# Performance work log

Hardware: AMD Instinct MI355X
Metric: run time of the kernel (lower is better)

Reference implementation:

```python
import jax, jax.numpy as jnp
import numpy as np

DOWNSAMPLE = 1

def _meshgrid(oh, ow):
    # grid rows: x in [-1,1] repeated per row, y in [-1,1] per column, ones -> [3, oh*ow]
    x_t = jnp.tile(jnp.linspace(-1.0, 1.0, ow, dtype=jnp.float32)[None, :], (oh, 1))
    y_t = jnp.tile(jnp.linspace(-1.0, 1.0, oh, dtype=jnp.float32)[:, None], (1, ow))
    ones = jnp.ones((1, oh * ow), dtype=jnp.float32)
    return jnp.concatenate([x_t.reshape(1, -1), y_t.reshape(1, -1), ones], axis=0)

def setup_inputs() -> dict:
    key = jax.random.key(0)
    k1, k2 = jax.random.split(key)
    B, C, H, W = 32, 16, 256, 256
    inp = jax.random.normal(k1, (B, C, H, W), dtype=jnp.float32)
    # theta near identity with noise so sampling is non-degenerate
    ident = jnp.array([1.0, 0.0, 0.0, 0.0, 1.0, 0.0], dtype=jnp.float32)
    theta = ident[None, :] + 0.1 * jax.random.normal(k2, (B, 6), dtype=jnp.float32)
    return {"input": inp, "theta": theta}

def reference(input, theta):
    B, C, H, W = input.shape
    oh, ow = H // DOWNSAMPLE, W // DOWNSAMPLE
    grid = _meshgrid(oh, ow)                      # [3, N] with N = oh*ow
    Tg = jnp.einsum('bij,jn->bin', theta.reshape(B, 2, 3), grid)  # [B,2,N]
    x = jnp.clip(Tg[:, 0], -1.0, 1.0)             # [B,N]
    y = jnp.clip(Tg[:, 1], -1.0, 1.0)
    x = (x + 1.0) * 0.5 * (W - 1)
    y = (y + 1.0) * 0.5 * (H - 1)
    x0f = jnp.floor(x); y0f = jnp.floor(y)
    x1f = x0f + 1.0;    y1f = y0f + 1.0
    x0 = x0f.astype(jnp.int32); y0 = y0f.astype(jnp.int32)
    x1 = jnp.minimum(x1f, W - 1).astype(jnp.int32)
    y1 = jnp.minimum(y1f, H - 1).astype(jnp.int32)
    im = jnp.transpose(input, (0, 2, 3, 1))        # [B,H,W,C] channels-last like the original
    b = jnp.arange(B, dtype=jnp.int32)[:, None]    # [B,1] broadcast over N
    Ia = im[b, y0, x0]                             # [B,N,C] four irregular gathers
    Ib = im[b, y1, x0]
    Ic = im[b, y0, x1]
    Id = im[b, y1, x1]
    wa = ((x1f - x) * (y1f - y))[..., None]
    wb = ((x1f - x) * (y - y0f))[..., None]
    wc = ((x - x0f) * (y1f - y))[..., None]
    wd = ((x - x0f) * (y - y0f))[..., None]
    out = wa * Ia + wb * Ib + wc * Ic + wd * Id    # [B,N,C]
    out = out.reshape(B, oh, ow, C)
    return jnp.transpose(out, (0, 3, 1, 2))        # [B,C,oh,ow]
```

## Files before the change

kernel.cpp:

```cpp
#include <hip/hip_runtime.h>

#define BB 32
#define CC 16
#define HH 256
#define WW 256
#define HWSZ (HH * WW)

#define TW 64
#define TH 16
#define NBLK (BB * (WW/TW) * (HH/TH))
#define NXCD 8

#define SROWS 48
#define SCOLS 100
#define MAXF4 25
#define KMAX 5

typedef float f2 __attribute__((ext_vector_type(2)));
typedef float f4 __attribute__((ext_vector_type(4)));

__global__ __launch_bounds__(256) void st_lds2_kernel(
    const float* __restrict__ input,
    const float* __restrict__ theta,
    float* __restrict__ out)
{
    __shared__ float S[SROWS * SCOLS];

    int bid = blockIdx.x;
    int wg = (bid & (NXCD - 1)) * (NBLK / NXCD) + (bid >> 3);

    int b  = wg >> 6;
    int r  = wg & 63;
    int yt = r >> 2;
    int xt = r & 3;

    int tid = threadIdx.x;
    int qy = tid >> 4;
    int qx = tid & 15;
    int oy  = yt * TH + qy;
    int oxb = xt * TW + qx * 4;

    const float* th = theta + b * 6;
    float t0 = th[0], t1 = th[1], t2 = th[2];
    float t3 = th[3], t4 = th[4], t5 = th[5];

    const float step = 2.0f / 255.0f;

    float gxa = -1.0f + (xt * TW) * step;
    float gxb = -1.0f + (xt * TW + TW - 1) * step;
    float gya = -1.0f + (yt * TH) * step;
    float gyb = -1.0f + (yt * TH + TH - 1) * step;

    float x00 = t0 * gxa + t1 * gya + t2, x01 = t0 * gxa + t1 * gyb + t2;
    float x10 = t0 * gxb + t1 * gya + t2, x11 = t0 * gxb + t1 * gyb + t2;
    float y00 = t3 * gxa + t4 * gya + t5, y01 = t3 * gxa + t4 * gyb + t5;
    float y10 = t3 * gxb + t4 * gya + t5, y11 = t3 * gxb + t4 * gyb + t5;

    float xmn = fminf(fminf(x00, x01), fminf(x10, x11));
    float xmx = fmaxf(fmaxf(x00, x01), fmaxf(x10, x11));
    float ymn = fminf(fminf(y00, y01), fminf(y10, y11));
    float ymx = fmaxf(fmaxf(y00, y01), fmaxf(y10, y11));
    xmn = fminf(fmaxf(xmn, -1.0f), 1.0f);
    xmx = fminf(fmaxf(xmx, -1.0f), 1.0f);
    ymn = fminf(fmaxf(ymn, -1.0f), 1.0f);
    ymx = fminf(fmaxf(ymx, -1.0f), 1.0f);
    float pxmn = (xmn + 1.0f) * 127.5f, pxmx = (xmx + 1.0f) * 127.5f;
    float pymn = (ymn + 1.0f) * 127.5f, pymx = (ymx + 1.0f) * 127.5f;

    int cx0 = (int)floorf(pxmn) - 2;
    cx0 = (max(0, min(cx0, WW - 4))) & ~3;
    int cxend = min((int)floorf(pxmx) + 3, WW - 1);
    int wf4 = (cxend - cx0 + 4) >> 2;
    wf4 = min(wf4, min(MAXF4, (WW - cx0) >> 2));
    int wcols = wf4 * 4;

    int ry0 = (int)floorf(pymn) - 2;
    ry0 = max(0, min(ry0, HH - 1));
    int ryend = min((int)floorf(pymx) + 3, HH - 1);
    int rows = min(min(ryend - ry0 + 1, SROWS), HH - ry0);
    int nf4 = rows * wf4;

    int  sg[KMAX], sl[KMAX];
    bool sv[KMAX];
    #pragma unroll
    for (int k = 0; k < KMAX; ++k) {
        int idx = tid + k * 256;
        sv[k] = idx < nf4;
        int rr = idx / wf4;
        int cq = idx - rr * wf4;
        sg[k] = rr * WW + cq * 4;
        sl[k] = rr * SCOLS + cq * 4;
    }

    int   off[4], goff[4];
    float w00[4], w01[4], w10[4], w11[4];
    bool  ok[4];
    float gy = -1.0f + oy * step;
    float cxp = t1 * gy + t2;
    float cyp = t4 * gy + t5;

    #pragma unroll
    for (int j = 0; j < 4; ++j) {
        float gx = -1.0f + (oxb + j) * step;
        float xs = fminf(fmaxf(t0 * gx + cxp, -1.0f), 1.0f);
        float ys = fminf(fmaxf(t3 * gx + cyp, -1.0f), 1.0f);
        float x = (xs + 1.0f) * 127.5f;
        float y = (ys + 1.0f) * 127.5f;
        float bxf = fminf(floorf(x), 254.0f);
        float byf = fminf(floorf(y), 254.0f);
        float fx = x - bxf, fy = y - byf;
        int bx = (int)bxf, by = (int)byf;

        w00[j] = (1.0f - fx) * (1.0f - fy);
        w01[j] = fx * (1.0f - fy);
        w10[j] = (1.0f - fx) * fy;
        w11[j] = fx * fy;

        int lx = bx - cx0, ly = by - ry0;
        ok[j] = (lx >= 0) && (lx <= wcols - 2) && (ly >= 0) && (ly <= rows - 2);
        off[j]  = ly * SCOLS + lx;
        goff[j] = by * WW + bx;
    }

    const float* ibase = input + (size_t)b * CC * HWSZ;
    float* obase = out + (size_t)b * CC * HWSZ + (size_t)oy * WW + oxb;

    for (int c = 0; c < CC; ++c) {
        __syncthreads();
        const float* src = ibase + c * HWSZ + ry0 * WW + cx0;
        #pragma unroll
        for (int k = 0; k < KMAX; ++k) {
            if (sv[k]) {
                *(f4*)&S[sl[k]] = *(const f4*)(src + sg[k]);
            }
        }
        __syncthreads();

        const float* p = ibase + c * HWSZ;
        f4 ov;
        #pragma unroll
        for (int j = 0; j < 4; ++j) {
            float v00, v01, v10, v11;
            if (ok[j]) {
                v00 = S[off[j]];
                v01 = S[off[j] + 1];
                v10 = S[off[j] + SCOLS];
                v11 = S[off[j] + SCOLS + 1];
            } else {
                f2 a, bb;
                __builtin_memcpy(&a,  p + goff[j], 8);
                __builtin_memcpy(&bb, p + goff[j] + WW, 8);
                v00 = a.x; v01 = a.y; v10 = bb.x; v11 = bb.y;
            }
            ov[j] = v00 * w00[j] + v01 * w01[j] + v10 * w10[j] + v11 * w11[j];
        }
        __builtin_nontemporal_store(ov, (f4*)(obase + c * HWSZ));
    }
}

extern "C" void kernel_launch(void* const* d_in, const int* in_sizes, int n_in,
                              void* d_out, int out_size, void* d_ws, size_t ws_size,
                              hipStream_t stream) {
    const float* input = (const float*)d_in[0];
    const float* theta = (const float*)d_in[1];
    float* out = (float*)d_out;

    dim3 block(256);
    dim3 grid(NBLK);
    hipLaunchKernelGGL(st_lds2_kernel, grid, block, 0, stream,
                       input, theta, out);
}
```

Before: 55.13 us.

## Double-buffer LDS tile and prefetch next channel into registers

```diff
diff --git a/kernel.cpp b/kernel.cpp
--- a/kernel.cpp
+++ b/kernel.cpp
@@ -11,20 +11,20 @@
 #define NBLK (BB * (WW/TW) * (HH/TH))
 #define NXCD 8
 
-#define SROWS 48
-#define SCOLS 100
+#define SROWS 39
+#define SCOLS 101
 #define MAXF4 25
-#define KMAX 5
+#define KMAX 4
 
 typedef float f2 __attribute__((ext_vector_type(2)));
 typedef float f4 __attribute__((ext_vector_type(4)));
 
-__global__ __launch_bounds__(256) void st_lds2_kernel(
+__global__ __launch_bounds__(256) void st_lds4_kernel(
     const float* __restrict__ input,
     const float* __restrict__ theta,
     float* __restrict__ out)
 {
-    __shared__ float S[SROWS * SCOLS];
+    __shared__ float S[2][SROWS * SCOLS];
 
     int bid = blockIdx.x;
     int wg = (bid & (NXCD - 1)) * (NBLK / NXCD) + (bid >> 3);
@@ -67,16 +67,16 @@
     float pxmn = (xmn + 1.0f) * 127.5f, pxmx = (xmx + 1.0f) * 127.5f;
     float pymn = (ymn + 1.0f) * 127.5f, pymx = (ymx + 1.0f) * 127.5f;
 
-    int cx0 = (int)floorf(pxmn) - 2;
+    int cx0 = (int)floorf(pxmn) - 1;
     cx0 = (max(0, min(cx0, WW - 4))) & ~3;
-    int cxend = min((int)floorf(pxmx) + 3, WW - 1);
+    int cxend = min((int)floorf(pxmx) + 2, WW - 1);
     int wf4 = (cxend - cx0 + 4) >> 2;
     wf4 = min(wf4, min(MAXF4, (WW - cx0) >> 2));
     int wcols = wf4 * 4;
 
-    int ry0 = (int)floorf(pymn) - 2;
+    int ry0 = (int)floorf(pymn) - 1;
     ry0 = max(0, min(ry0, HH - 1));
-    int ryend = min((int)floorf(pymx) + 3, HH - 1);
+    int ryend = min((int)floorf(pymx) + 2, HH - 1);
     int rows = min(min(ryend - ry0 + 1, SROWS), HH - ry0);
     int nf4 = rows * wf4;
 
@@ -125,16 +125,34 @@
     const float* ibase = input + (size_t)b * CC * HWSZ;
     float* obase = out + (size_t)b * CC * HWSZ + (size_t)oy * WW + oxb;
 
+    f4 rbuf[KMAX];
+    {
+        const float* src = ibase + ry0 * WW + cx0;
+        #pragma unroll
+        for (int k = 0; k < KMAX; ++k)
+            if (sv[k]) rbuf[k] = *(const f4*)(src + sg[k]);
+    }
+
+    #pragma unroll
     for (int c = 0; c < CC; ++c) {
-        __syncthreads();
-        const float* src = ibase + c * HWSZ + ry0 * WW + cx0;
+        float* Sb = &S[c & 1][0];
         #pragma unroll
         for (int k = 0; k < KMAX; ++k) {
             if (sv[k]) {
-                *(f4*)&S[sl[k]] = *(const f4*)(src + sg[k]);
+                Sb[sl[k]]     = rbuf[k].x;
+                Sb[sl[k] + 1] = rbuf[k].y;
+                Sb[sl[k] + 2] = rbuf[k].z;
+                Sb[sl[k] + 3] = rbuf[k].w;
             }
         }
         __syncthreads();
+
+        if (c + 1 < CC) {
+            const float* src = ibase + (c + 1) * HWSZ + ry0 * WW + cx0;
+            #pragma unroll
+            for (int k = 0; k < KMAX; ++k)
+                if (sv[k]) rbuf[k] = *(const f4*)(src + sg[k]);
+        }
 
         const float* p = ibase + c * HWSZ;
         f4 ov;
@@ -142,10 +160,10 @@
         for (int j = 0; j < 4; ++j) {
             float v00, v01, v10, v11;
             if (ok[j]) {
-                v00 = S[off[j]];
-                v01 = S[off[j] + 1];
-                v10 = S[off[j] + SCOLS];
-                v11 = S[off[j] + SCOLS + 1];
+                v00 = Sb[off[j]];
+                v01 = Sb[off[j] + 1];
+                v10 = Sb[off[j] + SCOLS];
+                v11 = Sb[off[j] + SCOLS + 1];
             } else {
                 f2 a, bb;
                 __builtin_memcpy(&a,  p + goff[j], 8);
@@ -167,6 +185,6 @@
 
     dim3 block(256);
     dim3 grid(NBLK);
-    hipLaunchKernelGGL(st_lds2_kernel, grid, block, 0, stream,
+    hipLaunchKernelGGL(st_lds4_kernel, grid, block, 0, stream,
                        input, theta, out);
 }
```

After: 68.38 us. 24.0% more time.
